# Optimization experiments

Hardware: AMD Instinct MI355X
Metric: run time of the kernel (lower is better)

## Reference

```python
import jax, jax.numpy as jnp
import numpy as np

EPS = 1e-15


def _cdist(a, b):
    # batched euclidean pairwise distance, a:[B,N,K] b:[B,M,K] -> [B,N,M]
    d2 = (jnp.sum(a * a, -1)[:, :, None] + jnp.sum(b * b, -1)[:, None, :]
          - 2.0 * jnp.einsum('bik,bjk->bij', a, b))
    return jnp.sqrt(jnp.maximum(d2, 0.0))


def _rank3_diag(d_flat):
    # [B,N] -> [B,N,N] diagonal
    eye = jnp.eye(d_flat.shape[1], dtype=d_flat.dtype)
    return eye * d_flat[:, :, None]


def _trace(m):
    return jnp.einsum('bjj->b', m)


def dense_ct_rewiring(x, adj, s, mask):
    s = jnp.tanh(s)
    m = mask[:, :, None].astype(x.dtype)
    x = x * m
    s = s * m
    k = s.shape[-1]
    d_flat = jnp.sum(adj, axis=-1)              # [B,N]
    d = _rank3_diag(d_flat) + EPS               # EPS added to full matrix (faithful to torch)
    L = d - adj
    out_adj = jnp.einsum('bnk,bnm,bml->bkl', s, L, s)
    ct_num = _trace(out_adj)
    ct_den = _trace(jnp.einsum('bnk,bnm,bml->bkl', s, d, s)) + EPS
    ct_dist = _cdist(s, s)                      # [B,N,N]
    vol = _trace(d)                             # [B]
    ct_dist = ct_dist / vol[:, None, None]
    adj_new = ct_dist * adj
    ct_loss = jnp.mean(ct_num / ct_den)
    ss = jnp.einsum('bnk,bnl->bkl', s, s)
    i_s = jnp.eye(k, dtype=ss.dtype)
    ss_n = jnp.sqrt(jnp.sum(ss * ss, axis=(-1, -2), keepdims=True))
    diff = ss / ss_n - i_s
    ortho_loss = jnp.sqrt(jnp.sum(diff * diff))  # global Frobenius norm, mean of scalar
    return adj_new, ct_loss, ortho_loss


def dense_mincut_pool(x, adj, s, mask):
    s = jax.nn.softmax(s, axis=-1)
    m = mask[:, :, None].astype(x.dtype)
    x = x * m
    s = s * m
    k = s.shape[-1]
    out = jnp.einsum('bnk,bnf->bkf', s, x)
    out_adj = jnp.einsum('bnk,bnm,bml->bkl', s, adj, s)
    mincut_num = _trace(out_adj)
    d_flat = jnp.sum(adj, axis=-1) + EPS
    d = _rank3_diag(d_flat)
    mincut_den = _trace(jnp.einsum('bnk,bnm,bml->bkl', s, d, s))
    mincut_loss = jnp.mean(-(mincut_num / mincut_den))
    ss = jnp.einsum('bnk,bnl->bkl', s, s)
    i_s = jnp.eye(k, dtype=ss.dtype)
    ss_n = jnp.sqrt(jnp.sum(ss * ss, axis=(-1, -2), keepdims=True))
    diff = ss / ss_n - i_s / jnp.sqrt(jnp.asarray(float(k), ss.dtype))
    ortho_loss = jnp.mean(jnp.sqrt(jnp.sum(diff * diff, axis=(-1, -2))))
    # zero diagonal, then symmetric degree normalization
    out_adj = out_adj * (1.0 - i_s)
    dk = jnp.sqrt(jnp.sum(out_adj, axis=-1) + EPS) + EPS  # [B,k]
    out_adj = out_adj / dk[:, None, :] / dk[:, :, None]
    return out, out_adj, mincut_loss, ortho_loss


def dense_graph_conv(x, adj, w_rel, b_rel, w_root):
    # PyG DenseGraphConv(aggr='add'): lin_rel(adj @ x) + lin_root(x)
    return jnp.matmul(jnp.matmul(adj, x), w_rel) + b_rel + jnp.matmul(x, w_root)


def ctnet_forward(x, adj, mask,
                  W_lin1, b_lin1, W_pool1, b_pool1, W_pool2, b_pool2,
                  Wrel1, brel1, Wroot1, Wrel2, brel2, Wroot2,
                  W_lin2, b_lin2, W_lin3, b_lin3):
    x = jnp.matmul(x, W_lin1) + b_lin1
    s1 = jnp.matmul(x, W_pool1) + b_pool1
    adj, ct_loss, ortho1 = dense_ct_rewiring(x, adj, s1, mask)
    x = dense_graph_conv(x, adj, Wrel1, brel1, Wroot1)
    s2 = jnp.matmul(x, W_pool2) + b_pool2
    x, adj, mincut2, ortho2 = dense_mincut_pool(x, adj, s2, mask)
    x = dense_graph_conv(x, adj, Wrel2, brel2, Wroot2)
    x = jnp.sum(x, axis=1)
    x = jax.nn.relu(jnp.matmul(x, W_lin2) + b_lin2)
    x = jnp.matmul(x, W_lin3) + b_lin3
    return jax.nn.log_softmax(x, axis=-1), ct_loss + ortho1, mincut2 + ortho2


def _init_lin(key, fan_in, fan_out):
    k1, k2 = jax.random.split(key)
    lim = 1.0 / np.sqrt(fan_in)
    W = jax.random.uniform(k1, (fan_in, fan_out), jnp.float32, -lim, lim)
    b = jax.random.uniform(k2, (fan_out,), jnp.float32, -lim, lim)
    return W, b


def setup_inputs() -> dict:
    key = jax.random.key(0)
    ks = jax.random.split(key, 12)
    B, N, Fin, H, K, OUT, K2 = 16, 1024, 128, 32, 64, 10, 16
    x = jax.random.normal(ks[0], (B, N, Fin), jnp.float32)
    adj = jax.random.uniform(ks[1], (B, N, N), jnp.float32)
    mask = jnp.ones((B, N), jnp.bool_)
    W_lin1, b_lin1 = _init_lin(ks[2], Fin, H)
    W_pool1, b_pool1 = _init_lin(ks[3], H, K)
    W_pool2, b_pool2 = _init_lin(ks[4], H, K2)
    Wrel1, brel1 = _init_lin(ks[5], H, H)
    Wroot1, _ = _init_lin(ks[6], H, H)
    Wrel2, brel2 = _init_lin(ks[7], H, H)
    Wroot2, _ = _init_lin(ks[8], H, H)
    W_lin2, b_lin2 = _init_lin(ks[9], H, H)
    W_lin3, b_lin3 = _init_lin(ks[10], H, OUT)
    return dict(x=x, adj=adj, mask=mask,
                W_lin1=W_lin1, b_lin1=b_lin1, W_pool1=W_pool1, b_pool1=b_pool1,
                W_pool2=W_pool2, b_pool2=b_pool2,
                Wrel1=Wrel1, brel1=brel1, Wroot1=Wroot1,
                Wrel2=Wrel2, brel2=brel2, Wroot2=Wroot2,
                W_lin2=W_lin2, b_lin2=b_lin2, W_lin3=W_lin3, b_lin3=b_lin3)


def reference(x, adj, mask,
              W_lin1, b_lin1, W_pool1, b_pool1, W_pool2, b_pool2,
              Wrel1, brel1, Wroot1, Wrel2, brel2, Wroot2,
              W_lin2, b_lin2, W_lin3, b_lin3):
    return ctnet_forward(x, adj, mask,
                         W_lin1, b_lin1, W_pool1, b_pool1, W_pool2, b_pool2,
                         Wrel1, brel1, Wroot1, Wrel2, brel2, Wroot2,
                         W_lin2, b_lin2, W_lin3, b_lin3)
```

## Files before the change

### kernel.cpp

```cpp
#include <hip/hip_runtime.h>

typedef unsigned short u16;
typedef unsigned int   u32;
typedef __attribute__((ext_vector_type(8))) short bf16x8;
typedef __attribute__((ext_vector_type(4))) float f32x4;

#define EPSF 1e-15f

__device__ __forceinline__ float* accp(float* xb, int b, int a) {
    return xb + (size_t)(b*1024 + a/14)*128 + 114 + (a % 14);
}

__device__ __forceinline__ float bf2f(u16 u) {
    union { u32 i; float f; } v; v.i = ((u32)u) << 16; return v.f;
}
__device__ __forceinline__ u16 f2bf(float f) {
    union { u32 i; float f; } v; v.f = f;
    u32 r = v.i + 0x7fffu + ((v.i >> 16) & 1u);
    return (u16)(r >> 16);
}

__global__ __launch_bounds__(256) void k_a(float* xb,
        const float* __restrict__ W1, const float* __restrict__ b1,
        const float* __restrict__ Wp1, const float* __restrict__ bp1)
{
    __shared__ float W1s[128*32];
    __shared__ float Wp1s[32*64];
    __shared__ float xs[16][128];
    __shared__ float x1s[16][32];
    int tid = threadIdx.x;
    for (int i = tid; i < 1024; i += 256)
        *(float4*)&W1s[i*4] = *(const float4*)&W1[i*4];
    for (int i = tid; i < 512; i += 256)
        *(float4*)&Wp1s[i*4] = *(const float4*)&Wp1[i*4];
    int rbase = blockIdx.x*16;
    for (int e = tid; e < 512; e += 256) {
        int rr = e >> 5, c = e & 31;
        *(float4*)&xs[rr][c*4] = *(const float4*)&xb[(size_t)(rbase + rr)*128 + c*4];
    }
    __syncthreads();
    int w = tid >> 6, l = tid & 63;
    int col = l & 31, half = l >> 5;
    #pragma unroll
    for (int i = 0; i < 4; ++i) {
        int rr = w*4 + i;
        float* xr = xb + (size_t)(rbase + rr)*128;
        if (l == 33) xr[96] = 0.f;
        if (l < 15) xr[113 + l] = 0.f;
        float acc = half ? 0.f : b1[col];
        const float* xrow = &xs[rr][half*64];
        const float* wrow = &W1s[half*64*32 + col];
        for (int f = 0; f < 64; ++f) acc += xrow[f]*wrow[f*32];
        acc += __shfl_down(acc, 32);
        if (l < 32) x1s[rr][l] = acc;
    }
    __syncthreads();
    #pragma unroll
    for (int i = 0; i < 4; ++i) {
        int rr = w*4 + i;
        float* xr = xb + (size_t)(rbase + rr)*128;
        if (l < 32) xr[64 + l] = x1s[rr][l];
        float acc = bp1[l];
        for (int h = 0; h < 32; ++h) acc += x1s[rr][h]*Wp1s[h*64 + l];
        float sv = tanhf(acc);
        u32 me = (u32)f2bf(sv);
        u32 nb = __shfl_down(me, 1);
        if (!(l & 1)) ((u32*)xr)[l >> 1] = me | (nb << 16);
        float svr = bf2f((u16)me);
        float qv = svr*svr;
        for (int off = 32; off; off >>= 1) qv += __shfl_down(qv, off);
        if (l == 0) xr[112] = qv;
    }
}

__global__ __launch_bounds__(256, 8) void k_c(const float* __restrict__ adj, float* xb,
                                              u32* __restrict__ anb)
{
    __shared__ __align__(16) u32 SMEM[64*36];
    __shared__ __align__(16) float qBs[64];
    __shared__ float pw[2][4];
    int tid = threadIdx.x;
    int tj = blockIdx.x, ti = blockIdx.y, b = blockIdx.z;
    int w = tid >> 6, lane = tid & 63;
    int q = lane >> 4, c16 = lane & 15;
    int rloc = w*16 + c16;
    size_t rowg = (size_t)(b*1024 + ti*64 + rloc);
    const u32* xu = (const u32*)xb;
    float4 a4s[4];
    #pragma unroll
    for (int t = 0; t < 4; ++t)
        a4s[t] = *(const float4*)&adj[rowg*1024 + tj*64 + t*16 + q*4];
    bf16x8 bfr0 = *(const bf16x8*)&xu[rowg*128 + q*4];
    bf16x8 bfr1 = *(const bf16x8*)&xu[rowg*128 + 16 + q*4];
    float qa = xb[rowg*128 + 112];
    u16* BufB = (u16*)SMEM;
    for (int e = tid; e < 512; e += 256) {
        int n = e >> 3, c = e & 7;
        *(float4*)&BufB[n*72 + c*8] =
            *(const float4*)&xu[(size_t)(b*1024 + tj*64 + n)*128 + c*4];
    }
    if (tid < 64) qBs[tid] = xb[(size_t)(b*1024 + tj*64 + tid)*128 + 112];
    __syncthreads();
    f32x4 g[4];
    #pragma unroll
    for (int t = 0; t < 4; ++t) {
        bf16x8 af0 = *(const bf16x8*)&BufB[(t*16 + c16)*72 + q*8];
        bf16x8 af1 = *(const bf16x8*)&BufB[(t*16 + c16)*72 + 32 + q*8];
        f32x4 gg = {0.f, 0.f, 0.f, 0.f};
        gg = __builtin_amdgcn_mfma_f32_16x16x32_bf16(af0, bfr0, gg, 0, 0, 0);
        gg = __builtin_amdgcn_mfma_f32_16x16x32_bf16(af1, bfr1, gg, 0, 0, 0);
        g[t] = gg;
    }
    __syncthreads();
    float dsum = 0.f, rsum = 0.f, Pt = 0.f, Qt = 0.f;
    #pragma unroll
    for (int t = 0; t < 4; ++t) {
        float4 a4 = a4s[t];
        float4 qb4 = *(const float4*)&qBs[t*16 + q*4];
        float av[4] = {a4.x, a4.y, a4.z, a4.w};
        float qb[4] = {qb4.x, qb4.y, qb4.z, qb4.w};
        float o[4];
        #pragma unroll
        for (int rg = 0; rg < 4; ++rg) {
            float d2v = qa + qb[rg] - 2.f*g[t][rg];
            float dist = sqrtf(fmaxf(d2v, 0.f));
            o[rg] = dist * av[rg];
            dsum += av[rg];
            rsum += o[rg];
            Pt += av[rg]*g[t][rg];
            Qt += g[t][rg]*g[t][rg];
        }
        u32 p0 = (u32)f2bf(o[0]) | ((u32)f2bf(o[1]) << 16);
        u32 p1 = (u32)f2bf(o[2]) | ((u32)f2bf(o[3]) << 16);
        *(uint2*)&SMEM[rloc*34 + t*8 + q*2] = make_uint2(p0, p1);
    }
    rsum += __shfl_xor(rsum, 16); rsum += __shfl_xor(rsum, 32);
    dsum += __shfl_xor(dsum, 16); dsum += __shfl_xor(dsum, 32);
    if (q == 0) {
        atomicAdd(&xb[rowg*128 + 96],  dsum);
        atomicAdd(&xb[rowg*128 + 113], rsum);
    }
    for (int off = 32; off; off >>= 1) { Pt += __shfl_down(Pt, off); Qt += __shfl_down(Qt, off); }
    if (lane == 0) { pw[0][w] = Pt; pw[1][w] = Qt; }
    __syncthreads();
    {
        int row = tid >> 2, c8 = (tid & 3)*8;
        uint4 v0 = *(const uint4*)&SMEM[row*34 + c8];
        uint4 v1 = *(const uint4*)&SMEM[row*34 + c8 + 4];
        size_t go = (size_t)(b*1024 + ti*64 + row)*512 + tj*32 + c8;
        *(uint4*)&anb[go]     = v0;
        *(uint4*)&anb[go + 4] = v1;
    }
    if (tid == 0) {
        atomicAdd(accp(xb,b,3), pw[0][0]+pw[0][1]+pw[0][2]+pw[0][3]);
        atomicAdd(accp(xb,b,4), pw[1][0]+pw[1][1]+pw[1][2]+pw[1][3]);
    }
}

__global__ __launch_bounds__(256) void k_y(const u32* __restrict__ anb, float* xb)
{
    __shared__ __align__(16) u16 X[16*1032];
    int tid = threadIdx.x;
    int hq = blockIdx.x, ni = blockIdx.y, b = blockIdx.z;
    int w = tid >> 6, lane = tid & 63;
    int q = lane >> 4, c16 = lane & 15;
    int rloc = w*16 + c16;
    size_t rowg = (size_t)(b*1024 + ni*64 + rloc);
    u32* Xu = (u32*)X;
    for (int e = tid; e < 2048; e += 256) {
        int mp = e >> 2, h4 = e & 3;
        int m0 = mp*2;
        const float* p0 = &xb[(size_t)(b*1024 + m0)*128 + 64 + hq*16 + h4*4];
        float4 v0 = *(const float4*)p0;
        float4 v1 = *(const float4*)(p0 + 128);
        Xu[(h4*4 + 0)*516 + mp] = (u32)f2bf(v0.x) | ((u32)f2bf(v1.x) << 16);
        Xu[(h4*4 + 1)*516 + mp] = (u32)f2bf(v0.y) | ((u32)f2bf(v1.y) << 16);
        Xu[(h4*4 + 2)*516 + mp] = (u32)f2bf(v0.z) | ((u32)f2bf(v1.z) << 16);
        Xu[(h4*4 + 3)*516 + mp] = (u32)f2bf(v0.w) | ((u32)f2bf(v1.w) << 16);
    }
    __syncthreads();
    f32x4 acc = {0.f,0.f,0.f,0.f};
    #pragma unroll 8
    for (int ks = 0; ks < 32; ++ks) {
        bf16x8 af = *(const bf16x8*)&anb[rowg*512 + ks*16 + q*4];
        bf16x8 bx = *(const bf16x8*)&X[c16*1032 + ks*32 + q*8];
        acc = __builtin_amdgcn_mfma_f32_16x16x32_bf16(af, bx, acc, 0, 0, 0);
    }
    #pragma unroll
    for (int rg = 0; rg < 4; ++rg) {
        size_t orow = (size_t)(b*1024 + ni*64 + w*16 + q*4 + rg)*128;
        xb[orow + 32 + hq*16 + c16] = acc[rg];
    }
    if (hq == 0 && tid < 64) {
        const float* xr = xb + (size_t)(b*1024 + ni*64 + tid)*128;
        float d = xr[96], qv = xr[112];
        float t0 = d, t1 = d*qv, t2 = qv;
        for (int off = 32; off; off >>= 1) {
            t0 += __shfl_down(t0, off); t1 += __shfl_down(t1, off); t2 += __shfl_down(t2, off);
        }
        if (tid == 0) {
            atomicAdd(accp(xb,b,0), t0);
            atomicAdd(accp(xb,b,1), t1);
            atomicAdd(accp(xb,b,2), t2);
        }
    }
}

__global__ __launch_bounds__(256) void k_d2(float* xb,
        const float* __restrict__ Wrel1, const float* __restrict__ brel1,
        const float* __restrict__ Wroot1,
        const float* __restrict__ Wp2, const float* __restrict__ bp2)
{
    __shared__ float ys[32*34];
    __shared__ float x1n[32*34];
    __shared__ float x2s[32*34];
    __shared__ float s2s[32*17];
    __shared__ float Wr[1024], Wo[1024], Wp[512];
    __shared__ float pwd[4];
    int tid = threadIdx.x;
    int tq = blockIdx.x, b = blockIdx.y;
    int rbase = b*1024 + tq*32;
    float invv = 1.f / (*accp(xb,b,0) + 1024.f*EPSF);
    for (int i = tid; i < 1024; i += 256) { Wr[i] = Wrel1[i]; Wo[i] = Wroot1[i]; }
    for (int i = tid; i < 512; i += 256) Wp[i] = Wp2[i];
    for (int e = tid; e < 1024; e += 256) {
        int r = e >> 5, h = e & 31;
        const float* xr = xb + (size_t)(rbase + r)*128;
        ys[r*34 + h]  = xr[32 + h] * invv;
        x1n[r*34 + h] = xr[64 + h];
    }
    __syncthreads();
    {
        int h = tid & 31, tg = tid >> 5;
        float brl = brel1[h];
        #pragma unroll
        for (int i = 0; i < 4; ++i) {
            int r = tg + 8*i;
            float v = brl;
            for (int j = 0; j < 32; ++j)
                v += ys[r*34 + j]*Wr[j*32 + h] + x1n[r*34 + j]*Wo[j*32 + h];
            x2s[r*34 + h] = v;
        }
    }
    __syncthreads();
    {
        int rl = tid & 7, kq = (tid >> 3) & 7, wv = tid >> 6;
        int r = wv*8 + rl;
        int k0 = kq*2;
        float v0 = bp2[k0], v1 = bp2[k0 + 1];
        for (int j = 0; j < 32; ++j) {
            float xv = x2s[r*34 + j];
            v0 += xv*Wp[j*16 + k0];
            v1 += xv*Wp[j*16 + k0 + 1];
        }
        float mx = fmaxf(v0, v1);
        mx = fmaxf(mx, __shfl_xor(mx, 8));
        mx = fmaxf(mx, __shfl_xor(mx, 16));
        mx = fmaxf(mx, __shfl_xor(mx, 32));
        float e0 = expf(v0 - mx), e1 = expf(v1 - mx);
        float sm = e0 + e1;
        sm += __shfl_xor(sm, 8); sm += __shfl_xor(sm, 16); sm += __shfl_xor(sm, 32);
        float inv = 1.f/sm;
        float sv0 = e0*inv, sv1 = e1*inv;
        s2s[r*17 + k0]     = sv0;
        s2s[r*17 + k0 + 1] = sv1;
        ((u32*)(xb + (size_t)(rbase + r)*128))[kq] =
            (u32)f2bf(sv0) | ((u32)f2bf(sv1) << 16);
        float q2v = sv0*sv0 + sv1*sv1;
        q2v += __shfl_xor(q2v, 8); q2v += __shfl_xor(q2v, 16); q2v += __shfl_xor(q2v, 32);
        float denp = (kq == 0)
            ? (xb[(size_t)(rbase + r)*128 + 113]*invv + EPSF)*q2v : 0.f;
        denp += __shfl_down(denp, 1);
        denp += __shfl_down(denp, 2);
        denp += __shfl_down(denp, 4);
        if ((tid & 63) == 0) pwd[wv] = denp;
    }
    __syncthreads();
    if (tid == 0) atomicAdd(accp(xb,b,5), pwd[0]+pwd[1]+pwd[2]+pwd[3]);
    {
        int k = tid >> 4, l = tid & 15;
        float s = 0.f;
        for (int r = 0; r < 32; ++r) s += s2s[r*17 + k]*s2s[r*17 + l];
        atomicAdd(accp(xb,b,774 + tid), s);
    }
    for (int e = tid; e < 512; e += 256) {
        int k = e >> 5, h = e & 31;
        float s = 0.f;
        for (int r = 0; r < 32; ++r) s += s2s[r*17 + k]*x2s[r*34 + h];
        atomicAdd(accp(xb,b,6 + k*32 + h), s);
    }
}

__global__ __launch_bounds__(256) void k_e(const u32* __restrict__ anb, float* xb)
{
    __shared__ __align__(16) u16 BufS[2][16*72];
    __shared__ __align__(16) u16 BufN[16*72];
    __shared__ __align__(16) u16 zT[16*72];
    int tid = threadIdx.x;
    int miq = blockIdx.x, ni = blockIdx.y, b = blockIdx.z;
    const u32* xu = (const u32*)xb;
    for (int e = tid; e < 512; e += 256) {
        int node = e >> 3, lw = e & 7;
        u32 pp = xu[(size_t)(b*1024 + ni*64 + node)*128 + lw];
        BufN[(lw*2)*72 + node]     = (u16)pp;
        BufN[(lw*2 + 1)*72 + node] = (u16)(pp >> 16);
    }
    for (int e = tid; e < 1024; e += 256) {
        int t = e >> 9, e2 = e & 511;
        int node = e2 >> 3, lw = e2 & 7;
        u32 pp = xu[(size_t)(b*1024 + (miq*2 + t)*64 + node)*128 + lw];
        BufS[t][(lw*2)*72 + node]     = (u16)pp;
        BufS[t][(lw*2 + 1)*72 + node] = (u16)(pp >> 16);
    }
    int w = tid >> 6, lane = tid & 63;
    int q = lane >> 4, c16 = lane & 15;
    int rloc = w*16 + c16;
    size_t arow = (size_t)(b*1024 + ni*64 + rloc)*512;
    bf16x8 ya[2][2];
    #pragma unroll
    for (int t = 0; t < 2; ++t) {
        ya[t][0] = *(const bf16x8*)&anb[arow + (miq*2 + t)*32 + q*4];
        ya[t][1] = *(const bf16x8*)&anb[arow + (miq*2 + t)*32 + 16 + q*4];
    }
    __syncthreads();
    f32x4 zacc = {0.f, 0.f, 0.f, 0.f};
    #pragma unroll
    for (int t = 0; t < 2; ++t) {
        bf16x8 yb0 = *(const bf16x8*)&BufS[t][c16*72 + q*8];
        bf16x8 yb1 = *(const bf16x8*)&BufS[t][c16*72 + 32 + q*8];
        zacc = __builtin_amdgcn_mfma_f32_16x16x32_bf16(ya[t][0], yb0, zacc, 0, 0, 0);
        zacc = __builtin_amdgcn_mfma_f32_16x16x32_bf16(ya[t][1], yb1, zacc, 0, 0, 0);
    }
    #pragma unroll
    for (int rg = 0; rg < 4; ++rg)
        zT[c16*72 + w*16 + q*4 + rg] = f2bf(zacc[rg]);
    __syncthreads();
    if (w == 0) {
        bf16x8 af0 = *(const bf16x8*)&BufN[c16*72 + q*8];
        bf16x8 af1 = *(const bf16x8*)&BufN[c16*72 + 32 + q*8];
        bf16x8 bz0 = *(const bf16x8*)&zT[c16*72 + q*8];
        bf16x8 bz1 = *(const bf16x8*)&zT[c16*72 + 32 + q*8];
        f32x4 oamv = {0.f, 0.f, 0.f, 0.f};
        oamv = __builtin_amdgcn_mfma_f32_16x16x32_bf16(af0, bz0, oamv, 0, 0, 0);
        oamv = __builtin_amdgcn_mfma_f32_16x16x32_bf16(af1, bz1, oamv, 0, 0, 0);
        #pragma unroll
        for (int rg = 0; rg < 4; ++rg)
            atomicAdd(accp(xb, b, 518 + (q*4 + rg)*16 + c16), oamv[rg]);
    }
}

__global__ __launch_bounds__(256) void k_f1(float* xb,
        const float* __restrict__ Wrel2, const float* __restrict__ brel2,
        const float* __restrict__ Wroot2,
        const float* __restrict__ W_lin2, const float* __restrict__ b_lin2,
        const float* __restrict__ W_lin3, const float* __restrict__ b_lin3,
        float* __restrict__ outp)
{
    __shared__ float oam_s[256], ssm_s[256], outm_s[512];
    __shared__ float dks[16], csoa[16];
    __shared__ float cs0[32], cs1[32], xsum[32], x5[32], lgs[10];
    __shared__ float red[4];
    __shared__ int isLast;
    int b = blockIdx.x;
    int tid = threadIdx.x;
    float invv = 1.f / (*accp(xb,b,0) + 1024.f*EPSF);
    oam_s[tid] = *accp(xb,b,518 + tid) * invv;
    ssm_s[tid] = *accp(xb,b,774 + tid);
    for (int e = tid; e < 512; e += 256) outm_s[e] = *accp(xb,b,6 + e);
    __syncthreads();
    if (tid < 16) {
        float rsv = 0.f;
        for (int l = 0; l < 16; ++l) if (l != tid) rsv += oam_s[tid*16 + l];
        dks[tid] = sqrtf(fmaxf(rsv, 0.f) + EPSF) + EPSF;
    }
    {
        float v = ssm_s[tid];
        float p = v*v;
        for (int off = 32; off; off >>= 1) p += __shfl_down(p, off);
        if ((tid & 63) == 0) red[tid >> 6] = p;
    }
    __syncthreads();
    if (tid < 16) {
        float s = 0.f;
        for (int k2 = 0; k2 < 16; ++k2)
            if (k2 != tid) s += oam_s[k2*16 + tid] / dks[k2];
        csoa[tid] = s / dks[tid];
    }
    if (tid < 32) {
        float s0 = 0.f, s1 = 0.f;
        for (int l = 0; l < 16; ++l) {
            float ov = outm_s[l*32 + tid];
            s0 += ov;
            s1 += csoa[l] * ov;
        }
        cs0[tid] = s0; cs1[tid] = s1;
    }
    if (tid == 64) {
        float T1v  = *accp(xb,b,1);
        float Pgv  = *accp(xb,b,3);
        float Q2v  = *accp(xb,b,4);
        float Tq1v = *accp(xb,b,2);
        float T2v  = *accp(xb,b,5);
        float tr2 = 0.f, trs = 0.f;
        for (int k2 = 0; k2 < 16; ++k2) { tr2 += oam_s[k2*17]; trs += ssm_s[k2*17]; }
        float fr2 = red[0] + red[1] + red[2] + red[3];
        __hip_atomic_store(accp(xb,b,1030), (T1v - Pgv) / (T1v + EPSF),
                           __ATOMIC_RELAXED, __HIP_MEMORY_SCOPE_AGENT);
        __hip_atomic_store(accp(xb,b,1031), 65.f - 2.f*Tq1v/sqrtf(fmaxf(Q2v, 1e-30f)),
                           __ATOMIC_RELAXED, __HIP_MEMORY_SCOPE_AGENT);
        __hip_atomic_store(accp(xb,b,1032), -tr2 / T2v,
                           __ATOMIC_RELAXED, __HIP_MEMORY_SCOPE_AGENT);
        __hip_atomic_store(accp(xb,b,1033),
                           sqrtf(fmaxf(2.f - trs/(2.f*sqrtf(fmaxf(fr2, 1e-30f))), 0.f)),
                           __ATOMIC_RELAXED, __HIP_MEMORY_SCOPE_AGENT);
    }
    __syncthreads();
    if (tid < 32) {
        float v = 16.f * brel2[tid];
        for (int j = 0; j < 32; ++j)
            v += cs1[j]*Wrel2[j*32 + tid] + cs0[j]*Wroot2[j*32 + tid];
        xsum[tid] = v;
    }
    __syncthreads();
    if (tid < 32) {
        float v = b_lin2[tid];
        for (int j = 0; j < 32; ++j) v += xsum[j]*W_lin2[j*32 + tid];
        x5[tid] = fmaxf(v, 0.f);
    }
    __syncthreads();
    if (tid < 10) {
        float v = b_lin3[tid];
        for (int j = 0; j < 32; ++j) v += x5[j]*W_lin3[j*10 + tid];
        lgs[tid] = v;
    }
    __syncthreads();
    if (tid < 10) {
        float mx = -1e30f;
        for (int t = 0; t < 10; ++t) mx = fmaxf(mx, lgs[t]);
        float sum = 0.f;
        for (int t = 0; t < 10; ++t) sum += expf(lgs[t] - mx);
        outp[b*10 + tid] = lgs[tid] - mx - logf(sum);
    }
    __syncthreads();
    if (tid == 0) {
        __threadfence();
        float old = atomicAdd(accp(xb,0,1035), 1.f);
        isLast = (old > 14.5f) ? 1 : 0;
    }
    __syncthreads();
    if (isLast && tid < 64) {
        __threadfence();
        int b2 = tid & 15, which = tid >> 4;
        float v = __hip_atomic_load(accp(xb,b2,1030 + which),
                                    __ATOMIC_RELAXED, __HIP_MEMORY_SCOPE_AGENT);
        for (int off = 1; off < 16; off <<= 1) v += __shfl_xor(v, off);
        float ct = __shfl(v, 0);
        float o1 = __shfl(v, 16);
        float mc = __shfl(v, 32);
        float o2 = __shfl(v, 48);
        if (tid == 0) {
            outp[160] = ct/16.f + sqrtf(fmaxf(o1, 0.f));
            outp[161] = mc/16.f + o2/16.f;
        }
    }
}

extern "C" void kernel_launch(void* const* d_in, const int* in_sizes, int n_in,
                              void* d_out, int out_size, void* d_ws, size_t ws_size,
                              hipStream_t stream)
{
    float* xb        = (float*)d_in[0];
    const float* adj = (const float*)d_in[1];
    const float* W_lin1 = (const float*)d_in[3];
    const float* b_lin1 = (const float*)d_in[4];
    const float* W_pool1= (const float*)d_in[5];
    const float* b_pool1= (const float*)d_in[6];
    const float* W_pool2= (const float*)d_in[7];
    const float* b_pool2= (const float*)d_in[8];
    const float* Wrel1  = (const float*)d_in[9];
    const float* brel1  = (const float*)d_in[10];
    const float* Wroot1 = (const float*)d_in[11];
    const float* Wrel2  = (const float*)d_in[12];
    const float* brel2  = (const float*)d_in[13];
    const float* Wroot2 = (const float*)d_in[14];
    const float* W_lin2 = (const float*)d_in[15];
    const float* b_lin2 = (const float*)d_in[16];
    const float* W_lin3 = (const float*)d_in[17];
    const float* b_lin3 = (const float*)d_in[18];
    u32* anb = (u32*)d_ws;
    (void)ws_size; (void)in_sizes; (void)n_in; (void)out_size;

    k_a<<<dim3(1024),      dim3(256), 0, stream>>>(xb, W_lin1, b_lin1, W_pool1, b_pool1);
    k_c<<<dim3(16,16,16),  dim3(256), 0, stream>>>(adj, xb, anb);
    k_y<<<dim3(2,16,16),   dim3(256), 0, stream>>>(anb, xb);
    k_d2<<<dim3(32,16),    dim3(256), 0, stream>>>(xb, Wrel1, brel1, Wroot1,
                                                   W_pool2, b_pool2);
    k_e<<<dim3(8,16,16),   dim3(256), 0, stream>>>(anb, xb);
    k_f1<<<dim3(16),       dim3(256), 0, stream>>>(xb, Wrel2, brel2, Wroot2,
                                                   W_lin2, b_lin2, W_lin3, b_lin3,
                                                   (float*)d_out);
}
```

Measured before the change: 244.8 us.

## Process two column tiles per k_c block and transpose small weight tiles in shared memory

k_c now handles two 64-column tiles per block. The A-side bf16 fragment and its norms are staged once in shared memory and reused across both tiles, which halves the grid and lowers occupancy bounds from 8 to 5. The output adjacency is written straight to global in 8-byte pieces instead of going through a shared-memory transpose for 16-byte stores. In k_a and k_d2 the weight matrices are stored transposed with padding so each thread reads contiguous rows. This may change LDS bank-conflict behaviour and gives up some store coalescing in exchange.

```diff
diff --git a/kernel.cpp b/kernel.cpp
--- a/kernel.cpp
+++ b/kernel.cpp
@@ -24,15 +24,27 @@
         const float* __restrict__ W1, const float* __restrict__ b1,
         const float* __restrict__ Wp1, const float* __restrict__ bp1)
 {
-    __shared__ float W1s[128*32];
-    __shared__ float Wp1s[32*64];
+    __shared__ float W1sT[32*133];
+    __shared__ float Wp1sT[64*33];
     __shared__ float xs[16][128];
     __shared__ float x1s[16][32];
     int tid = threadIdx.x;
-    for (int i = tid; i < 1024; i += 256)
-        *(float4*)&W1s[i*4] = *(const float4*)&W1[i*4];
-    for (int i = tid; i < 512; i += 256)
-        *(float4*)&Wp1s[i*4] = *(const float4*)&Wp1[i*4];
+    for (int i = tid; i < 1024; i += 256) {
+        int f = i >> 3, c0 = (i & 7)*4;
+        float4 v = *(const float4*)&W1[f*32 + c0];
+        W1sT[(c0+0)*133 + f] = v.x;
+        W1sT[(c0+1)*133 + f] = v.y;
+        W1sT[(c0+2)*133 + f] = v.z;
+        W1sT[(c0+3)*133 + f] = v.w;
+    }
+    for (int i = tid; i < 512; i += 256) {
+        int h = i >> 4, l0 = (i & 15)*4;
+        float4 v = *(const float4*)&Wp1[h*64 + l0];
+        Wp1sT[(l0+0)*33 + h] = v.x;
+        Wp1sT[(l0+1)*33 + h] = v.y;
+        Wp1sT[(l0+2)*33 + h] = v.z;
+        Wp1sT[(l0+3)*33 + h] = v.w;
+    }
     int rbase = blockIdx.x*16;
     for (int e = tid; e < 512; e += 256) {
         int rr = e >> 5, c = e & 31;
@@ -49,8 +61,8 @@
         if (l < 15) xr[113 + l] = 0.f;
         float acc = half ? 0.f : b1[col];
         const float* xrow = &xs[rr][half*64];
-        const float* wrow = &W1s[half*64*32 + col];
-        for (int f = 0; f < 64; ++f) acc += xrow[f]*wrow[f*32];
+        const float* wrow = &W1sT[col*133 + half*64];
+        for (int f = 0; f < 64; ++f) acc += xrow[f]*wrow[f];
         acc += __shfl_down(acc, 32);
         if (l < 32) x1s[rr][l] = acc;
     }
@@ -61,7 +73,8 @@
         float* xr = xb + (size_t)(rbase + rr)*128;
         if (l < 32) xr[64 + l] = x1s[rr][l];
         float acc = bp1[l];
-        for (int h = 0; h < 32; ++h) acc += x1s[rr][h]*Wp1s[h*64 + l];
+        const float* wp = &Wp1sT[l*33];
+        for (int h = 0; h < 32; ++h) acc += x1s[rr][h]*wp[h];
         float sv = tanhf(acc);
         u32 me = (u32)f2bf(sv);
         u32 nb = __shfl_down(me, 1);
@@ -73,66 +86,80 @@
     }
 }
 
-__global__ __launch_bounds__(256, 8) void k_c(const float* __restrict__ adj, float* xb,
+__global__ __launch_bounds__(256, 5) void k_c(const float* __restrict__ adj, float* xb,
                                               u32* __restrict__ anb)
 {
-    __shared__ __align__(16) u32 SMEM[64*36];
-    __shared__ __align__(16) float qBs[64];
+    __shared__ __align__(16) u16 BufA[64*72];
+    __shared__ __align__(16) u16 BufB[2][64*72];
+    __shared__ __align__(16) float qAs[64], qBs[2][64];
     __shared__ float pw[2][4];
     int tid = threadIdx.x;
-    int tj = blockIdx.x, ti = blockIdx.y, b = blockIdx.z;
+    int tjq = blockIdx.x, ti = blockIdx.y, b = blockIdx.z;
     int w = tid >> 6, lane = tid & 63;
     int q = lane >> 4, c16 = lane & 15;
     int rloc = w*16 + c16;
     size_t rowg = (size_t)(b*1024 + ti*64 + rloc);
+    float4 a4s[2][4];
+    #pragma unroll
+    for (int tt = 0; tt < 2; ++tt)
+        #pragma unroll
+        for (int t = 0; t < 4; ++t)
+            a4s[tt][t] = *(const float4*)&adj[rowg*1024 + (tjq*2 + tt)*64 + t*16 + q*4];
     const u32* xu = (const u32*)xb;
-    float4 a4s[4];
-    #pragma unroll
-    for (int t = 0; t < 4; ++t)
-        a4s[t] = *(const float4*)&adj[rowg*1024 + tj*64 + t*16 + q*4];
-    bf16x8 bfr0 = *(const bf16x8*)&xu[rowg*128 + q*4];
-    bf16x8 bfr1 = *(const bf16x8*)&xu[rowg*128 + 16 + q*4];
-    float qa = xb[rowg*128 + 112];
-    u16* BufB = (u16*)SMEM;
     for (int e = tid; e < 512; e += 256) {
         int n = e >> 3, c = e & 7;
-        *(float4*)&BufB[n*72 + c*8] =
-            *(const float4*)&xu[(size_t)(b*1024 + tj*64 + n)*128 + c*4];
-    }
-    if (tid < 64) qBs[tid] = xb[(size_t)(b*1024 + tj*64 + tid)*128 + 112];
-    __syncthreads();
-    f32x4 g[4];
-    #pragma unroll
-    for (int t = 0; t < 4; ++t) {
-        bf16x8 af0 = *(const bf16x8*)&BufB[(t*16 + c16)*72 + q*8];
-        bf16x8 af1 = *(const bf16x8*)&BufB[(t*16 + c16)*72 + 32 + q*8];
-        f32x4 gg = {0.f, 0.f, 0.f, 0.f};
-        gg = __builtin_amdgcn_mfma_f32_16x16x32_bf16(af0, bfr0, gg, 0, 0, 0);
-        gg = __builtin_amdgcn_mfma_f32_16x16x32_bf16(af1, bfr1, gg, 0, 0, 0);
-        g[t] = gg;
-    }
-    __syncthreads();
+        *(float4*)&BufA[n*72 + c*8] = *(const float4*)&xu[(size_t)(b*1024 + ti*64 + n)*128 + c*4];
+    }
+    for (int e = tid; e < 1024; e += 256) {
+        int n2 = e >> 3, c = e & 7;
+        int tt = n2 >> 6, n = n2 & 63;
+        *(float4*)&BufB[tt][n*72 + c*8] =
+            *(const float4*)&xu[(size_t)(b*1024 + (tjq*2 + tt)*64 + n)*128 + c*4];
+    }
+    if (tid < 64) qAs[tid] = xb[(size_t)(b*1024 + ti*64 + tid)*128 + 112];
+    else if (tid < 192) {
+        int t2 = tid - 64;
+        qBs[t2 >> 6][t2 & 63] =
+            xb[(size_t)(b*1024 + (tjq*2 + (t2 >> 6))*64 + (t2 & 63))*128 + 112];
+    }
+    __syncthreads();
+    bf16x8 bfr0 = *(const bf16x8*)&BufA[rloc*72 + q*8];
+    bf16x8 bfr1 = *(const bf16x8*)&BufA[rloc*72 + 32 + q*8];
+    float qa = qAs[rloc];
     float dsum = 0.f, rsum = 0.f, Pt = 0.f, Qt = 0.f;
     #pragma unroll
-    for (int t = 0; t < 4; ++t) {
-        float4 a4 = a4s[t];
-        float4 qb4 = *(const float4*)&qBs[t*16 + q*4];
-        float av[4] = {a4.x, a4.y, a4.z, a4.w};
-        float qb[4] = {qb4.x, qb4.y, qb4.z, qb4.w};
-        float o[4];
+    for (int tt = 0; tt < 2; ++tt) {
+        f32x4 g[4];
         #pragma unroll
-        for (int rg = 0; rg < 4; ++rg) {
-            float d2v = qa + qb[rg] - 2.f*g[t][rg];
-            float dist = sqrtf(fmaxf(d2v, 0.f));
-            o[rg] = dist * av[rg];
-            dsum += av[rg];
-            rsum += o[rg];
-            Pt += av[rg]*g[t][rg];
-            Qt += g[t][rg]*g[t][rg];
-        }
-        u32 p0 = (u32)f2bf(o[0]) | ((u32)f2bf(o[1]) << 16);
-        u32 p1 = (u32)f2bf(o[2]) | ((u32)f2bf(o[3]) << 16);
-        *(uint2*)&SMEM[rloc*34 + t*8 + q*2] = make_uint2(p0, p1);
+        for (int t = 0; t < 4; ++t) {
+            bf16x8 af0 = *(const bf16x8*)&BufB[tt][(t*16 + c16)*72 + q*8];
+            bf16x8 af1 = *(const bf16x8*)&BufB[tt][(t*16 + c16)*72 + 32 + q*8];
+            f32x4 gg = {0.f, 0.f, 0.f, 0.f};
+            gg = __builtin_amdgcn_mfma_f32_16x16x32_bf16(af0, bfr0, gg, 0, 0, 0);
+            gg = __builtin_amdgcn_mfma_f32_16x16x32_bf16(af1, bfr1, gg, 0, 0, 0);
+            g[t] = gg;
+        }
+        #pragma unroll
+        for (int t = 0; t < 4; ++t) {
+            float4 a4 = a4s[tt][t];
+            float4 qb4 = *(const float4*)&qBs[tt][t*16 + q*4];
+            float av[4] = {a4.x, a4.y, a4.z, a4.w};
+            float qb[4] = {qb4.x, qb4.y, qb4.z, qb4.w};
+            float o[4];
+            #pragma unroll
+            for (int rg = 0; rg < 4; ++rg) {
+                float d2v = qa + qb[rg] - 2.f*g[t][rg];
+                float dist = sqrtf(fmaxf(d2v, 0.f));
+                o[rg] = dist * av[rg];
+                dsum += av[rg];
+                rsum += o[rg];
+                Pt += av[rg]*g[t][rg];
+                Qt += g[t][rg]*g[t][rg];
+            }
+            u32 p0 = (u32)f2bf(o[0]) | ((u32)f2bf(o[1]) << 16);
+            u32 p1 = (u32)f2bf(o[2]) | ((u32)f2bf(o[3]) << 16);
+            *(uint2*)&anb[rowg*512 + (tjq*2 + tt)*32 + t*8 + q*2] = make_uint2(p0, p1);
+        }
     }
     rsum += __shfl_xor(rsum, 16); rsum += __shfl_xor(rsum, 32);
     dsum += __shfl_xor(dsum, 16); dsum += __shfl_xor(dsum, 32);
@@ -143,14 +170,6 @@
     for (int off = 32; off; off >>= 1) { Pt += __shfl_down(Pt, off); Qt += __shfl_down(Qt, off); }
     if (lane == 0) { pw[0][w] = Pt; pw[1][w] = Qt; }
     __syncthreads();
-    {
-        int row = tid >> 2, c8 = (tid & 3)*8;
-        uint4 v0 = *(const uint4*)&SMEM[row*34 + c8];
-        uint4 v1 = *(const uint4*)&SMEM[row*34 + c8 + 4];
-        size_t go = (size_t)(b*1024 + ti*64 + row)*512 + tj*32 + c8;
-        *(uint4*)&anb[go]     = v0;
-        *(uint4*)&anb[go + 4] = v1;
-    }
     if (tid == 0) {
         atomicAdd(accp(xb,b,3), pw[0][0]+pw[0][1]+pw[0][2]+pw[0][3]);
         atomicAdd(accp(xb,b,4), pw[1][0]+pw[1][1]+pw[1][2]+pw[1][3]);
@@ -215,14 +234,33 @@
     __shared__ float x1n[32*34];
     __shared__ float x2s[32*34];
     __shared__ float s2s[32*17];
-    __shared__ float Wr[1024], Wo[1024], Wp[512];
+    __shared__ float WrT[32*33], WoT[32*33], WpT[16*33];
     __shared__ float pwd[4];
     int tid = threadIdx.x;
     int tq = blockIdx.x, b = blockIdx.y;
     int rbase = b*1024 + tq*32;
     float invv = 1.f / (*accp(xb,b,0) + 1024.f*EPSF);
-    for (int i = tid; i < 1024; i += 256) { Wr[i] = Wrel1[i]; Wo[i] = Wroot1[i]; }
-    for (int i = tid; i < 512; i += 256) Wp[i] = Wp2[i];
+    {
+        int j = tid >> 3, h0 = (tid & 7)*4;
+        float4 v = *(const float4*)&Wrel1[j*32 + h0];
+        WrT[(h0+0)*33 + j] = v.x;
+        WrT[(h0+1)*33 + j] = v.y;
+        WrT[(h0+2)*33 + j] = v.z;
+        WrT[(h0+3)*33 + j] = v.w;
+        float4 v2 = *(const float4*)&Wroot1[j*32 + h0];
+        WoT[(h0+0)*33 + j] = v2.x;
+        WoT[(h0+1)*33 + j] = v2.y;
+        WoT[(h0+2)*33 + j] = v2.z;
+        WoT[(h0+3)*33 + j] = v2.w;
+    }
+    if (tid < 128) {
+        int j = tid >> 2, k0 = (tid & 3)*4;
+        float4 v = *(const float4*)&Wp2[j*16 + k0];
+        WpT[(k0+0)*33 + j] = v.x;
+        WpT[(k0+1)*33 + j] = v.y;
+        WpT[(k0+2)*33 + j] = v.z;
+        WpT[(k0+3)*33 + j] = v.w;
+    }
     for (int e = tid; e < 1024; e += 256) {
         int r = e >> 5, h = e & 31;
         const float* xr = xb + (size_t)(rbase + r)*128;
@@ -233,12 +271,14 @@
     {
         int h = tid & 31, tg = tid >> 5;
         float brl = brel1[h];
+        const float* wr = &WrT[h*33];
+        const float* wo = &WoT[h*33];
         #pragma unroll
         for (int i = 0; i < 4; ++i) {
             int r = tg + 8*i;
             float v = brl;
             for (int j = 0; j < 32; ++j)
-                v += ys[r*34 + j]*Wr[j*32 + h] + x1n[r*34 + j]*Wo[j*32 + h];
+                v += ys[r*34 + j]*wr[j] + x1n[r*34 + j]*wo[j];
             x2s[r*34 + h] = v;
         }
     }
@@ -248,10 +288,12 @@
         int r = wv*8 + rl;
         int k0 = kq*2;
         float v0 = bp2[k0], v1 = bp2[k0 + 1];
+        const float* wp0 = &WpT[k0*33];
+        const float* wp1 = &WpT[(k0+1)*33];
         for (int j = 0; j < 32; ++j) {
             float xv = x2s[r*34 + j];
-            v0 += xv*Wp[j*16 + k0];
-            v1 += xv*Wp[j*16 + k0 + 1];
+            v0 += xv*wp0[j];
+            v1 += xv*wp1[j];
         }
         float mx = fmaxf(v0, v1);
         mx = fmaxf(mx, __shfl_xor(mx, 8));
@@ -491,7 +533,7 @@
     (void)ws_size; (void)in_sizes; (void)n_in; (void)out_size;
 
     k_a<<<dim3(1024),      dim3(256), 0, stream>>>(xb, W_lin1, b_lin1, W_pool1, b_pool1);
-    k_c<<<dim3(16,16,16),  dim3(256), 0, stream>>>(adj, xb, anb);
+    k_c<<<dim3(8,16,16),   dim3(256), 0, stream>>>(adj, xb, anb);
     k_y<<<dim3(2,16,16),   dim3(256), 0, stream>>>(anb, xb);
     k_d2<<<dim3(32,16),    dim3(256), 0, stream>>>(xb, Wrel1, brel1, Wroot1,
                                                    W_pool2, b_pool2);
```

Result: faster. 220.2 us (-10.0%).
